# Optimization experiments

Hardware: AMD Instinct MI355X
Metric: run time of the kernel (lower is better)

The kernel has to match this reference:

```python
import jax, jax.numpy as jnp
import numpy as np
from itertools import combinations

B, F, C, MAX_ORDER = 4096, 32, 128, 3


def setup_inputs() -> dict:
    key = jax.random.key(0)
    ks = jax.random.split(key, 1 + MAX_ORDER)
    x = jax.random.normal(ks[0], (B, F), dtype=jnp.float32)
    # Exact combinatorial index lists, matching get_index_lists (all k-subsets, lexicographic)
    idx = [jnp.asarray(np.array(list(combinations(range(F), o)), dtype=np.int32))
           for o in range(1, MAX_ORDER + 1)]
    # Per-order Dense kernels [n_combos, num_classes] (glorot-ish scale), no bias (use_bias=False)
    Ws = [jax.random.normal(ks[i + 1], (idx[i].shape[0], C), dtype=jnp.float32)
          * (2.0 / (idx[i].shape[0] + C)) ** 0.5 for i in range(MAX_ORDER)]
    bias = jnp.zeros((1, C), dtype=jnp.float32)  # Zeros initializer
    return {"x": x, "bias": bias,
            "W1": Ws[0], "W2": Ws[1], "W3": Ws[2],
            "idx1": idx[0], "idx2": idx[1], "idx3": idx[2]}


def reference(x, bias, W1, W2, W3, idx1, idx2, idx3):
    # combine(): out = tile(bias) + sum_i Dense_i( prod over feature-subset of order i )
    out = jnp.broadcast_to(bias, (x.shape[0], bias.shape[1]))
    for idx, W in ((idx1, W1), (idx2, W2), (idx3, W3)):
        # x[:, idx]: [B, n_combos, order] gather; product over subset axis -> [B, n_combos]
        prods = jnp.prod(x[:, idx], axis=2)
        out = out + prods @ W  # [B, num_classes]
    return out
```

## Files before the change

### kernel.cpp

```cpp
#include <hip/hip_runtime.h>
#include <hip/hip_bf16.h>

constexpr int B_   = 4096;
constexpr int C_   = 128;
constexpr int K1   = 32;
constexpr int K2   = 496;
constexpr int K3   = 4960;
constexpr int KTOT = K1 + K2 + K3;
constexpr int NCH  = KTOT / 16;
constexpr int Q0 = 0, Q1 = 86, Q2 = 172, Q3 = 258, Q4 = NCH;

typedef __attribute__((ext_vector_type(8)))  short bf16x8;
typedef __attribute__((ext_vector_type(16))) float f32x16;

constexpr size_t WS_WT = 0;

struct Sched { short a[KTOT]; short b[KTOT]; short c[KTOT]; };
constexpr Sched make_sched() {
    Sched s{}; int k = 0;
    for (int i = 0; i < 32; ++i) { s.a[k] = i; s.b[k] = 32; s.c[k] = 32; ++k; }
    for (int i = 0; i < 32; ++i)
        for (int j = i + 1; j < 32; ++j) { s.a[k] = i; s.b[k] = j; s.c[k] = 32; ++k; }
    for (int i = 0; i < 32; ++i)
        for (int j = i + 1; j < 32; ++j)
            for (int l = j + 1; l < 32; ++l) { s.a[k] = i; s.b[k] = j; s.c[k] = l; ++k; }
    return s;
}
constexpr Sched SCH = make_sched();

template<int K>
__device__ __forceinline__ float prodK(const float (&xv)[33]) {
    return xv[SCH.a[K]] * xv[SCH.b[K]] * xv[SCH.c[K]];
}

template<int K0, int J>
__device__ __forceinline__ void prods8(const float (&xv)[33], bool hi, float (&q)[8]) {
    if constexpr (J < 8) {
        q[J] = hi ? prodK<K0 + 8 + J>(xv) : prodK<K0 + J>(xv);
        prods8<K0, J + 1>(xv, hi, q);
    }
}

template<int CH, int CHEND>
__device__ __forceinline__ void run_chunks(const float (&xv)[33], bool hi, int lane, int ct,
                                           const ushort* __restrict__ Wb, f32x16& acc) {
    if constexpr (CH < CHEND) {
        constexpr int K0 = CH * 16;
        bf16x8 b0 = *(const bf16x8*)(Wb + ((size_t)(CH * 4 + ct) * 64 + lane) * 8);
        float q[8];
        prods8<K0, 0>(xv, hi, q);
        union { ushort us[8]; bf16x8 v; } af;
        #pragma unroll
        for (int j = 0; j < 8; ++j) {
            __hip_bfloat16 h = __float2bfloat16(q[j]);
            af.us[j] = *reinterpret_cast<ushort*>(&h);
        }
        acc = __builtin_amdgcn_mfma_f32_32x32x16_bf16(af.v, b0, acc, 0, 0, 0);
        run_chunks<CH + 1, CHEND>(xv, hi, lane, ct, Wb, acc);
    }
}

__global__ __launch_bounds__(256)
void prep_wt(const float* __restrict__ W1,
             const float* __restrict__ W2,
             const float* __restrict__ W3,
             ushort* __restrict__ Wb)
{
    __shared__ ushort tile[16 * 130];
    const int gc = blockIdx.x, t = threadIdx.x;
    const int k0 = gc * 16;
    #pragma unroll
    for (int p = 0; p < 2; ++p) {
        int e  = p * 256 + t;
        int kk = e >> 5, cq = e & 31;
        int k  = k0 + kk;
        float4 v = {0.f, 0.f, 0.f, 0.f};
        if (k < K1)           v = ((const float4*)W1)[k * 32 + cq];
        else if (k < K1 + K2) v = ((const float4*)W2)[(k - K1) * 32 + cq];
        else if (k < KTOT)    v = ((const float4*)W3)[(k - K1 - K2) * 32 + cq];
        union { ushort u[4]; uint2 d; } o;
        __hip_bfloat16 h0 = __float2bfloat16(v.x); o.u[0] = *(ushort*)&h0;
        __hip_bfloat16 h1 = __float2bfloat16(v.y); o.u[1] = *(ushort*)&h1;
        __hip_bfloat16 h2 = __float2bfloat16(v.z); o.u[2] = *(ushort*)&h2;
        __hip_bfloat16 h3 = __float2bfloat16(v.w); o.u[3] = *(ushort*)&h3;
        *(uint2*)&tile[kk * 130 + cq * 4] = o.d;
    }
    __syncthreads();
    {
        int ct = t >> 6, lane = t & 63, n = lane & 31, kg = lane >> 5;
        union { ushort us[8]; uint4 d; } o;
        #pragma unroll
        for (int j = 0; j < 8; ++j) o.us[j] = tile[(kg * 8 + j) * 130 + ct * 32 + n];
        *(uint4*)&Wb[((size_t)(gc * 4 + ct) * 64 + lane) * 8] = o.d;
    }
}

__global__ __launch_bounds__(512, 2)
void poly_mfma(const float* __restrict__ x,
               const ushort* __restrict__ Wb,
               const float* __restrict__ bias,
               float* __restrict__ out)
{
    __shared__ float red[8][32 * 33];

    const int t    = threadIdx.x;
    const int lane = t & 63;
    const int w    = t >> 6;
    const int kq   = w & 3;
    const int rt   = w >> 2;
    const int m    = lane & 31;
    const bool hi  = lane >= 32;
    const int row0 = blockIdx.x * 64;
    const int ct   = blockIdx.y;

    float xv[33];
    {
        const float4* xrow = (const float4*)(x + (size_t)(row0 + rt * 32 + m) * 32);
        #pragma unroll
        for (int qv = 0; qv < 8; ++qv) {
            float4 v = xrow[qv];
            xv[qv * 4 + 0] = v.x; xv[qv * 4 + 1] = v.y;
            xv[qv * 4 + 2] = v.z; xv[qv * 4 + 3] = v.w;
        }
        xv[32] = 1.0f;
    }

    f32x16 acc;
    #pragma unroll
    for (int i = 0; i < 16; ++i) acc[i] = 0.f;

    switch (kq) {
        case 0:  run_chunks<Q0, Q1>(xv, hi, lane, ct, Wb, acc); break;
        case 1:  run_chunks<Q1, Q2>(xv, hi, lane, ct, Wb, acc); break;
        case 2:  run_chunks<Q2, Q3>(xv, hi, lane, ct, Wb, acc); break;
        default: run_chunks<Q3, Q4>(xv, hi, lane, ct, Wb, acc); break;
    }

    const int kg = hi ? 1 : 0;
    #pragma unroll
    for (int e = 0; e < 16; ++e) {
        int r = (e & 3) + 8 * (e >> 2) + 4 * kg;
        red[w][r * 33 + m] = acc[e];
    }
    __syncthreads();

    {
        int r  = t >> 3;
        int c0 = (t & 7) * 4;
        int rtile = r >> 5, rr = r & 31;
        float4 b = *(const float4*)&bias[ct * 32 + c0];
        float s[4] = {b.x, b.y, b.z, b.w};
        #pragma unroll
        for (int q = 0; q < 4; ++q)
            #pragma unroll
            for (int j = 0; j < 4; ++j)
                s[j] += red[rtile * 4 + q][rr * 33 + c0 + j];
        float4 o = {s[0], s[1], s[2], s[3]};
        *(float4*)&out[(size_t)(row0 + r) * C_ + ct * 32 + c0] = o;
    }
}

extern "C" void kernel_launch(void* const* d_in, const int* in_sizes, int n_in,
                              void* d_out, int out_size, void* d_ws, size_t ws_size,
                              hipStream_t stream)
{
    const float* x    = (const float*)d_in[0];
    const float* bias = (const float*)d_in[1];
    const float* W1   = (const float*)d_in[2];
    const float* W2   = (const float*)d_in[3];
    const float* W3   = (const float*)d_in[4];
    float* out = (float*)d_out;

    ushort* Wb = (ushort*)((char*)d_ws + WS_WT);

    prep_wt<<<NCH, 256, 0, stream>>>(W1, W2, W3, Wb);

    dim3 grid(B_ / 64, C_ / 32);
    poly_mfma<<<grid, 512, 0, stream>>>(x, Wb, bias, out);
}
```

Before: 82.65 us.

## Reuse A-fragment products across two column tiles per wave

```diff
diff --git a/kernel.cpp b/kernel.cpp
--- a/kernel.cpp
+++ b/kernel.cpp
@@ -8,7 +8,7 @@
 constexpr int K3   = 4960;
 constexpr int KTOT = K1 + K2 + K3;
 constexpr int NCH  = KTOT / 16;
-constexpr int Q0 = 0, Q1 = 86, Q2 = 172, Q3 = 258, Q4 = NCH;
+constexpr int E0=0, E1=43, E2=86, E3=129, E4=172, E5=215, E6=258, E7=301, E8=NCH;
 
 typedef __attribute__((ext_vector_type(8)))  short bf16x8;
 typedef __attribute__((ext_vector_type(16))) float f32x16;
@@ -42,11 +42,14 @@
 }
 
 template<int CH, int CHEND>
-__device__ __forceinline__ void run_chunks(const float (&xv)[33], bool hi, int lane, int ct,
-                                           const ushort* __restrict__ Wb, f32x16& acc) {
+__device__ __forceinline__ void run_chunks(const float (&xv)[33], bool hi, int lane, int ct0,
+                                           const ushort* __restrict__ Wb,
+                                           f32x16& acc0, f32x16& acc1) {
     if constexpr (CH < CHEND) {
         constexpr int K0 = CH * 16;
-        bf16x8 b0 = *(const bf16x8*)(Wb + ((size_t)(CH * 4 + ct) * 64 + lane) * 8);
+        const ushort* wp = Wb + ((size_t)(CH * 4 + ct0) * 64 + lane) * 8;
+        bf16x8 b0 = *(const bf16x8*)wp;
+        bf16x8 b1 = *(const bf16x8*)(wp + 64 * 8);
         float q[8];
         prods8<K0, 0>(xv, hi, q);
         union { ushort us[8]; bf16x8 v; } af;
@@ -55,8 +58,9 @@
             __hip_bfloat16 h = __float2bfloat16(q[j]);
             af.us[j] = *reinterpret_cast<ushort*>(&h);
         }
-        acc = __builtin_amdgcn_mfma_f32_32x32x16_bf16(af.v, b0, acc, 0, 0, 0);
-        run_chunks<CH + 1, CHEND>(xv, hi, lane, ct, Wb, acc);
+        acc0 = __builtin_amdgcn_mfma_f32_32x32x16_bf16(af.v, b0, acc0, 0, 0, 0);
+        acc1 = __builtin_amdgcn_mfma_f32_32x32x16_bf16(af.v, b1, acc1, 0, 0, 0);
+        run_chunks<CH + 1, CHEND>(xv, hi, lane, ct0, Wb, acc0, acc1);
     }
 }
 
@@ -101,21 +105,19 @@
                const float* __restrict__ bias,
                float* __restrict__ out)
 {
-    __shared__ float red[8][32 * 33];
+    __shared__ float red[8][32 * 66];
 
     const int t    = threadIdx.x;
     const int lane = t & 63;
     const int w    = t >> 6;
-    const int kq   = w & 3;
-    const int rt   = w >> 2;
     const int m    = lane & 31;
     const bool hi  = lane >= 32;
-    const int row0 = blockIdx.x * 64;
-    const int ct   = blockIdx.y;
+    const int row0 = blockIdx.x * 32;
+    const int ct0  = blockIdx.y * 2;
 
     float xv[33];
     {
-        const float4* xrow = (const float4*)(x + (size_t)(row0 + rt * 32 + m) * 32);
+        const float4* xrow = (const float4*)(x + (size_t)(row0 + m) * 32);
         #pragma unroll
         for (int qv = 0; qv < 8; ++qv) {
             float4 v = xrow[qv];
@@ -125,38 +127,42 @@
         xv[32] = 1.0f;
     }
 
-    f32x16 acc;
+    f32x16 acc0, acc1;
     #pragma unroll
-    for (int i = 0; i < 16; ++i) acc[i] = 0.f;
+    for (int i = 0; i < 16; ++i) { acc0[i] = 0.f; acc1[i] = 0.f; }
 
-    switch (kq) {
-        case 0:  run_chunks<Q0, Q1>(xv, hi, lane, ct, Wb, acc); break;
-        case 1:  run_chunks<Q1, Q2>(xv, hi, lane, ct, Wb, acc); break;
-        case 2:  run_chunks<Q2, Q3>(xv, hi, lane, ct, Wb, acc); break;
-        default: run_chunks<Q3, Q4>(xv, hi, lane, ct, Wb, acc); break;
+    switch (w) {
+        case 0:  run_chunks<E0, E1>(xv, hi, lane, ct0, Wb, acc0, acc1); break;
+        case 1:  run_chunks<E1, E2>(xv, hi, lane, ct0, Wb, acc0, acc1); break;
+        case 2:  run_chunks<E2, E3>(xv, hi, lane, ct0, Wb, acc0, acc1); break;
+        case 3:  run_chunks<E3, E4>(xv, hi, lane, ct0, Wb, acc0, acc1); break;
+        case 4:  run_chunks<E4, E5>(xv, hi, lane, ct0, Wb, acc0, acc1); break;
+        case 5:  run_chunks<E5, E6>(xv, hi, lane, ct0, Wb, acc0, acc1); break;
+        case 6:  run_chunks<E6, E7>(xv, hi, lane, ct0, Wb, acc0, acc1); break;
+        default: run_chunks<E7, E8>(xv, hi, lane, ct0, Wb, acc0, acc1); break;
     }
 
     const int kg = hi ? 1 : 0;
     #pragma unroll
     for (int e = 0; e < 16; ++e) {
         int r = (e & 3) + 8 * (e >> 2) + 4 * kg;
-        red[w][r * 33 + m] = acc[e];
+        red[w][r * 66 + m]      = acc0[e];
+        red[w][r * 66 + 32 + m] = acc1[e];
     }
     __syncthreads();
 
     {
-        int r  = t >> 3;
-        int c0 = (t & 7) * 4;
-        int rtile = r >> 5, rr = r & 31;
-        float4 b = *(const float4*)&bias[ct * 32 + c0];
+        int r  = t >> 4;
+        int c0 = (t & 15) * 4;
+        float4 b = *(const float4*)&bias[ct0 * 32 + c0];
         float s[4] = {b.x, b.y, b.z, b.w};
         #pragma unroll
-        for (int q = 0; q < 4; ++q)
+        for (int q = 0; q < 8; ++q)
             #pragma unroll
             for (int j = 0; j < 4; ++j)
-                s[j] += red[rtile * 4 + q][rr * 33 + c0 + j];
+                s[j] += red[q][r * 66 + c0 + j];
         float4 o = {s[0], s[1], s[2], s[3]};
-        *(float4*)&out[(size_t)(row0 + r) * C_ + ct * 32 + c0] = o;
+        *(float4*)&out[(size_t)(row0 + r) * C_ + ct0 * 32 + c0] = o;
     }
 }
 
@@ -175,6 +181,6 @@
 
     prep_wt<<<NCH, 256, 0, stream>>>(W1, W2, W3, Wb);
 
-    dim3 grid(B_ / 64, C_ / 32);
+    dim3 grid(B_ / 32, C_ / 64);
     poly_mfma<<<grid, 512, 0, stream>>>(x, Wb, bias, out);
 }
```

Result: slower. 86.70 us (+4.9%).
